# Kernel tuning notes

Measured on AMD Instinct MI355X. Metric: run time of the kernel, lower is better.

Reference implementation:

```python
import jax, jax.numpy as jnp
import numpy as np

N, M, FIN, FOUT, K = 16, 20000, 64, 64, 6
NNZ = 160000


def setup_inputs() -> dict:
    key = jax.random.key(0)
    k1, k2, k3, k4, k5, k6 = jax.random.split(key, 6)
    x = jax.random.normal(k1, (N, M, FIN), dtype=jnp.float32)
    # sparse Laplacian in COO form; small values keep the Chebyshev recurrence stable
    L_vals = jax.random.normal(k2, (NNZ,), dtype=jnp.float32) * 0.05
    L_rows = jax.random.randint(k3, (NNZ,), 0, M, dtype=jnp.int32)
    L_cols = jax.random.randint(k4, (NNZ,), 0, M, dtype=jnp.int32)
    stdv = 1.0 / np.sqrt(FOUT)
    weight = jax.random.uniform(k5, (FIN * K, FOUT), dtype=jnp.float32, minval=-stdv, maxval=stdv)
    bias = jax.random.uniform(k6, (FOUT,), dtype=jnp.float32, minval=-stdv, maxval=stdv)
    return {"x": x, "L_vals": L_vals, "weight": weight, "bias": bias,
            "L_rows": L_rows, "L_cols": L_cols}


def reference(x, L_vals, weight, bias, L_rows, L_cols):
    n, m, fin = x.shape
    # x0: [M, Fin*N], matching torch permute(1,2,0).view(M, Fin*N)
    x0 = jnp.transpose(x, (1, 2, 0)).reshape(m, fin * n)

    def spmm(v):  # sparse [M,M] @ dense [M, Fin*N]
        return jax.ops.segment_sum(L_vals[:, None] * v[L_cols], L_rows, num_segments=m)

    terms = [x0]
    if K > 1:
        x1 = spmm(x0)
        terms.append(x1)
    xk_2, xk_1 = x0, x1
    for _ in range(2, K):
        xk = 2.0 * spmm(xk_1) - xk_2
        terms.append(xk)
        xk_2, xk_1 = xk_1, xk

    xs = jnp.stack(terms, axis=0)                       # [K, M, Fin*N]
    xs = xs.reshape(K, m, fin, n)
    xs = jnp.transpose(xs, (3, 1, 2, 0)).reshape(n * m, fin * K)
    out = xs @ weight + bias                            # [N*M, Fout]
    return out.reshape(n, m, -1)
```

## Files before the change

### kernel.cpp

```cpp
#include <hip/hip_runtime.h>
#include <hip/hip_bf16.h>
#include <hip/hip_fp16.h>

#define NB 16
#define MB 20000
#define FINC 64
#define FOUTC 64
#define KCH 6
#define NNZC 160000
#define CW 1024
#define ELLW 32

typedef __attribute__((ext_vector_type(8))) short short8;
typedef __attribute__((ext_vector_type(4))) float float4v;
typedef __attribute__((ext_vector_type(4))) unsigned int ui4;

__device__ inline unsigned short f2bf(float f){
  unsigned int u = __float_as_uint(f);
  u += 0x7FFFu + ((u >> 16) & 1u);
  return (unsigned short)(u >> 16);
}
__device__ inline float bflo(unsigned int u){ return __uint_as_float(u << 16); }
__device__ inline float bfhi(unsigned int u){ return __uint_as_float(u & 0xFFFF0000u); }
__device__ inline float h2f(unsigned int bits){
  __half_raw hr; hr.x = (unsigned short)bits;
  return __half2float(*(__half*)&hr);
}

__global__ void k_build(const int* __restrict__ rows, const int* __restrict__ cols,
                        const float* __restrict__ vals,
                        int* __restrict__ cnt, unsigned int* __restrict__ ell){
  int i = blockIdx.x * 256 + threadIdx.x;
  if (i < NNZC){
    int r = rows[i];
    int slot = atomicAdd(&cnt[r], 1);
    if (slot < ELLW){
      __half h = __float2half(vals[i]);
      __half_raw hr = *(__half_raw*)&h;
      unsigned int entry = (unsigned int)(unsigned short)cols[i] | ((unsigned int)hr.x << 16);
      ell[r * ELLW + slot] = entry;
    }
  }
}

__global__ void __launch_bounds__(256) k_prep(const float* __restrict__ x,
                                              const float* __restrict__ w,
                                              unsigned short* __restrict__ G0,
                                              unsigned short* __restrict__ W2t){
  int b = blockIdx.x;
  if (b < 1250){
    int t = threadIdx.x;
    int m = b * 16 + (t >> 4);
    int fc = (t & 15) * 4;
    #pragma unroll
    for (int n = 0; n < NB; n++){
      float4 a = *(const float4*)(x + ((size_t)n * MB + m) * FINC + fc);
      unsigned short tmp[4] = {f2bf(a.x), f2bf(a.y), f2bf(a.z), f2bf(a.w)};
      *(uint2*)(G0 + (size_t)m * CW + n * FINC + fc) = *(const uint2*)tmp;
    }
  } else {
    int idx = (b - 1250) * 256 + threadIdx.x;
    if (idx < KCH * FINC * FOUTC){
      int k  = idx / (FINC * FOUTC);
      int fo = (idx / FINC) % FOUTC;
      int f  = idx % FINC;
      W2t[idx] = f2bf(w[(f * KCH + k) * FOUTC + fo]);
    }
  }
}

__device__ inline void gacc(float* acc, ui4 raw, float v){
  acc[0] += v * bflo(raw.x); acc[1] += v * bfhi(raw.x);
  acc[2] += v * bflo(raw.y); acc[3] += v * bfhi(raw.y);
  acc[4] += v * bflo(raw.z); acc[5] += v * bfhi(raw.z);
  acc[6] += v * bflo(raw.w); acc[7] += v * bfhi(raw.w);
}

__global__ void __launch_bounds__(128) k_spmm(const unsigned short* __restrict__ Gin,
                                              const unsigned short* __restrict__ Gprev,
                                              unsigned short* __restrict__ Gout,
                                              const int* __restrict__ cnt,
                                              const unsigned int* __restrict__ ell,
                                              int first){
  int bid = blockIdx.x;
  int xcd   = bid & 7;
  int t2    = bid >> 3;
  int phase = t2 / 1250;
  int mg    = t2 - phase * 1250;
  int slab  = xcd + 8 * phase;
  int t = threadIdx.x;
  int m = mg * 16 + (t >> 3);
  int co = slab * 64 + (t & 7) * 8;
  int deg = cnt[m]; if (deg > ELLW) deg = ELLW;

  const ui4* ep4 = (const ui4*)(ell + m * ELLW);
  ui4 q0 = ep4[0];
  ui4 q1 = ep4[1];
  ui4 pr = (ui4){0u,0u,0u,0u};
  if (!first) pr = *(const ui4*)(Gprev + (size_t)m * CW + co);

  const unsigned short* gb = Gin + co;
  ui4 r0 = *(const ui4*)(gb + (size_t)(q0.x & 0xFFFFu) * CW);
  ui4 r1 = *(const ui4*)(gb + (size_t)(q0.y & 0xFFFFu) * CW);
  ui4 r2 = *(const ui4*)(gb + (size_t)(q0.z & 0xFFFFu) * CW);
  ui4 r3 = *(const ui4*)(gb + (size_t)(q0.w & 0xFFFFu) * CW);
  ui4 r4 = *(const ui4*)(gb + (size_t)(q1.x & 0xFFFFu) * CW);
  ui4 r5 = *(const ui4*)(gb + (size_t)(q1.y & 0xFFFFu) * CW);
  ui4 r6 = *(const ui4*)(gb + (size_t)(q1.z & 0xFFFFu) * CW);
  ui4 r7 = *(const ui4*)(gb + (size_t)(q1.w & 0xFFFFu) * CW);

  float acc[8] = {0.f,0.f,0.f,0.f,0.f,0.f,0.f,0.f};
  gacc(acc, r0, h2f(q0.x >> 16));
  gacc(acc, r1, h2f(q0.y >> 16));
  gacc(acc, r2, h2f(q0.z >> 16));
  gacc(acc, r3, h2f(q0.w >> 16));
  gacc(acc, r4, h2f(q1.x >> 16));
  gacc(acc, r5, h2f(q1.y >> 16));
  gacc(acc, r6, h2f(q1.z >> 16));
  gacc(acc, r7, h2f(q1.w >> 16));

  if (deg > 8){
    for (int e = 8; e < deg; e += 8){
      ui4 a0 = ep4[e >> 2];
      ui4 a1 = ep4[(e >> 2) + 1];
      ui4 s0 = *(const ui4*)(gb + (size_t)(a0.x & 0xFFFFu) * CW);
      ui4 s1 = *(const ui4*)(gb + (size_t)(a0.y & 0xFFFFu) * CW);
      ui4 s2 = *(const ui4*)(gb + (size_t)(a0.z & 0xFFFFu) * CW);
      ui4 s3 = *(const ui4*)(gb + (size_t)(a0.w & 0xFFFFu) * CW);
      ui4 s4 = *(const ui4*)(gb + (size_t)(a1.x & 0xFFFFu) * CW);
      ui4 s5 = *(const ui4*)(gb + (size_t)(a1.y & 0xFFFFu) * CW);
      ui4 s6 = *(const ui4*)(gb + (size_t)(a1.z & 0xFFFFu) * CW);
      ui4 s7 = *(const ui4*)(gb + (size_t)(a1.w & 0xFFFFu) * CW);
      gacc(acc, s0, h2f(a0.x >> 16));
      gacc(acc, s1, h2f(a0.y >> 16));
      gacc(acc, s2, h2f(a0.z >> 16));
      gacc(acc, s3, h2f(a0.w >> 16));
      gacc(acc, s4, h2f(a1.x >> 16));
      gacc(acc, s5, h2f(a1.y >> 16));
      gacc(acc, s6, h2f(a1.z >> 16));
      gacc(acc, s7, h2f(a1.w >> 16));
    }
  }

  if (!first){
    float pv[8] = {bflo(pr.x), bfhi(pr.x), bflo(pr.y), bfhi(pr.y),
                   bflo(pr.z), bfhi(pr.z), bflo(pr.w), bfhi(pr.w)};
    #pragma unroll
    for (int i = 0; i < 8; i++) acc[i] = 2.f * acc[i] - pv[i];
  }
  unsigned short o[8];
  #pragma unroll
  for (int i = 0; i < 8; i++) o[i] = f2bf(acc[i]);
  *(ui4*)(Gout + (size_t)m * CW + co) = *(const ui4*)o;
}

#define LDA 72
__global__ void __launch_bounds__(256, 2) k_gemm(const unsigned short* __restrict__ G,
                                                 const unsigned short* __restrict__ W2t,
                                                 const float* __restrict__ bias,
                                                 float* __restrict__ out){
  __shared__ unsigned short la[128 * LDA];
  __shared__ unsigned short lb[FOUTC * LDA];
  int tid  = threadIdx.x;
  int wave = tid >> 6, lane = tid & 63;
  int quad = lane >> 4, l16 = lane & 15;
  int mblk = blockIdx.x;
  const size_t gsz = (size_t)MB * CW;

  float4v acc[2][4];
  #pragma unroll
  for (int i = 0; i < 2; i++)
    #pragma unroll
    for (int j = 0; j < 4; j++) acc[i][j] = (float4v){0.f, 0.f, 0.f, 0.f};

  const unsigned short* a0p = G + (size_t)mblk * 8 * CW;
  uint4 ra0 = *(const uint4*)(a0p + (0 * 256 + tid) * 8);
  uint4 ra1 = *(const uint4*)(a0p + (1 * 256 + tid) * 8);
  uint4 ra2 = *(const uint4*)(a0p + (2 * 256 + tid) * 8);
  uint4 ra3 = *(const uint4*)(a0p + (3 * 256 + tid) * 8);
  uint4 rb0 = *(const uint4*)(W2t + (0 * 256 + tid) * 8);
  uint4 rb1 = *(const uint4*)(W2t + (1 * 256 + tid) * 8);

  for (int k = 0; k < KCH; k++){
    __syncthreads();
    {
      int e0;
      e0 = (0 * 256 + tid) * 8; *(uint4*)(&la[(e0 >> 6) * LDA + (e0 & 63)]) = ra0;
      e0 = (1 * 256 + tid) * 8; *(uint4*)(&la[(e0 >> 6) * LDA + (e0 & 63)]) = ra1;
      e0 = (2 * 256 + tid) * 8; *(uint4*)(&la[(e0 >> 6) * LDA + (e0 & 63)]) = ra2;
      e0 = (3 * 256 + tid) * 8; *(uint4*)(&la[(e0 >> 6) * LDA + (e0 & 63)]) = ra3;
      e0 = (0 * 256 + tid) * 8; *(uint4*)(&lb[(e0 >> 6) * LDA + (e0 & 63)]) = rb0;
      e0 = (1 * 256 + tid) * 8; *(uint4*)(&lb[(e0 >> 6) * LDA + (e0 & 63)]) = rb1;
    }
    __syncthreads();
    int kn = (k + 1 < KCH) ? k + 1 : k;
    const unsigned short* an = G + (size_t)kn * gsz + (size_t)mblk * 8 * CW;
    const unsigned short* bn = W2t + kn * (FINC * FOUTC);
    uint4 na0 = *(const uint4*)(an + (0 * 256 + tid) * 8);
    uint4 na1 = *(const uint4*)(an + (1 * 256 + tid) * 8);
    uint4 na2 = *(const uint4*)(an + (2 * 256 + tid) * 8);
    uint4 na3 = *(const uint4*)(an + (3 * 256 + tid) * 8);
    uint4 nb0 = *(const uint4*)(bn + (0 * 256 + tid) * 8);
    uint4 nb1 = *(const uint4*)(bn + (1 * 256 + tid) * 8);

    #pragma unroll
    for (int kc = 0; kc < 2; kc++){
      short8 af[2], bfr[4];
      #pragma unroll
      for (int rt = 0; rt < 2; rt++){
        int row = wave * 32 + rt * 16 + l16;
        af[rt] = *(const short8*)(&la[row * LDA + kc * 32 + quad * 8]);
      }
      #pragma unroll
      for (int ct = 0; ct < 4; ct++){
        int fo = ct * 16 + l16;
        bfr[ct] = *(const short8*)(&lb[fo * LDA + kc * 32 + quad * 8]);
      }
      #pragma unroll
      for (int rt = 0; rt < 2; rt++)
        #pragma unroll
        for (int ct = 0; ct < 4; ct++)
          acc[rt][ct] = __builtin_amdgcn_mfma_f32_16x16x32_bf16(af[rt], bfr[ct], acc[rt][ct], 0, 0, 0);
    }
    ra0 = na0; ra1 = na1; ra2 = na2; ra3 = na3; rb0 = nb0; rb1 = nb1;
  }
  #pragma unroll
  for (int ct = 0; ct < 4; ct++){
    int fo = ct * 16 + l16;
    float bv = bias[fo];
    #pragma unroll
    for (int rt = 0; rt < 2; rt++){
      #pragma unroll
      for (int reg = 0; reg < 4; reg++){
        int rloc = wave * 32 + rt * 16 + quad * 4 + reg;
        int r = mblk * 128 + rloc;
        int m = r >> 4, n = r & 15;
        out[((size_t)n * MB + m) * FOUTC + fo] = acc[rt][ct][reg] + bv;
      }
    }
  }
}

extern "C" void kernel_launch(void* const* d_in, const int* in_sizes, int n_in,
                              void* d_out, int out_size, void* d_ws, size_t ws_size,
                              hipStream_t stream){
  const float* x    = (const float*)d_in[0];
  const float* Lv   = (const float*)d_in[1];
  const float* w    = (const float*)d_in[2];
  const float* bias = (const float*)d_in[3];
  const int*   Lr   = (const int*)d_in[4];
  const int*   Lc   = (const int*)d_in[5];
  float* out = (float*)d_out;

  char* ws = (char*)d_ws;
  unsigned short* G   = (unsigned short*)ws;
  unsigned short* W2t = (unsigned short*)(ws + 245760000);
  int* cnt            = (int*)(ws + 245809152);
  unsigned int* ell = (unsigned int*)d_out;

  (void)hipMemsetAsync(cnt, 0, MB * sizeof(int), stream);
  (void)hipMemsetAsync(ell, 0, MB * ELLW * sizeof(unsigned int), stream);

  k_build<<<dim3((NNZC + 255) / 256), dim3(256), 0, stream>>>(Lr, Lc, Lv, cnt, ell);
  k_prep <<<dim3(1250 + 96), dim3(256), 0, stream>>>(x, w, G, W2t);

  const size_t gsz = (size_t)MB * CW;
  k_spmm<<<dim3(1250 * 16), dim3(128), 0, stream>>>(G, (const unsigned short*)nullptr, G + gsz,
                                                    cnt, ell, 1);
  for (int k = 2; k < KCH; k++)
    k_spmm<<<dim3(1250 * 16), dim3(128), 0, stream>>>(G + (size_t)(k - 1) * gsz, G + (size_t)(k - 2) * gsz,
                                                      G + (size_t)k * gsz, cnt, ell, 0);

  k_gemm<<<dim3(MB / 8), dim3(256), 0, stream>>>(G, W2t, bias, out);
}
```

Measured before the change: 397.3 us.

## Loop over column slabs per block in SpMM and stage ELL entries in LDS

The SpMM kernel drops from 20000 blocks (one per row group and column slab, with XCD-aware slab mapping) to 1250 blocks that each loop over all 16 column slabs. Each block loads its rows' ELL entries into shared memory once, pre-decoding byte offsets and fp16 values, so the index and value decode is amortised across slabs. The cost is far fewer blocks (1250 of 128 threads) and a serialised slab loop, which reduces parallelism and latency hiding. It also removes the XCD-based mapping that kept slabs local to L2.

```diff
diff --git a/kernel.cpp b/kernel.cpp
--- a/kernel.cpp
+++ b/kernel.cpp
@@ -82,76 +82,89 @@
                                               const int* __restrict__ cnt,
                                               const unsigned int* __restrict__ ell,
                                               int first){
-  int bid = blockIdx.x;
-  int xcd   = bid & 7;
-  int t2    = bid >> 3;
-  int phase = t2 / 1250;
-  int mg    = t2 - phase * 1250;
-  int slab  = xcd + 8 * phase;
-  int t = threadIdx.x;
-  int m = mg * 16 + (t >> 3);
-  int co = slab * 64 + (t & 7) * 8;
+  __shared__ unsigned int loff[16 * ELLW];
+  __shared__ float        lval[16 * ELLW];
+  int blk = blockIdx.x;
+  int t   = threadIdx.x;
+  int r   = t >> 3;
+  int m   = blk * 16 + r;
+  int cth = t & 7;
+
+  {
+    ui4 e = ((const ui4*)(ell + blk * 16 * ELLW))[t];
+    int base = t * 4;
+    loff[base + 0] = (e.x & 0xFFFFu) * (CW * 2); lval[base + 0] = h2f(e.x >> 16);
+    loff[base + 1] = (e.y & 0xFFFFu) * (CW * 2); lval[base + 1] = h2f(e.y >> 16);
+    loff[base + 2] = (e.z & 0xFFFFu) * (CW * 2); lval[base + 2] = h2f(e.z >> 16);
+    loff[base + 3] = (e.w & 0xFFFFu) * (CW * 2); lval[base + 3] = h2f(e.w >> 16);
+  }
   int deg = cnt[m]; if (deg > ELLW) deg = ELLW;
-
-  const ui4* ep4 = (const ui4*)(ell + m * ELLW);
-  ui4 q0 = ep4[0];
-  ui4 q1 = ep4[1];
-  ui4 pr = (ui4){0u,0u,0u,0u};
-  if (!first) pr = *(const ui4*)(Gprev + (size_t)m * CW + co);
-
-  const unsigned short* gb = Gin + co;
-  ui4 r0 = *(const ui4*)(gb + (size_t)(q0.x & 0xFFFFu) * CW);
-  ui4 r1 = *(const ui4*)(gb + (size_t)(q0.y & 0xFFFFu) * CW);
-  ui4 r2 = *(const ui4*)(gb + (size_t)(q0.z & 0xFFFFu) * CW);
-  ui4 r3 = *(const ui4*)(gb + (size_t)(q0.w & 0xFFFFu) * CW);
-  ui4 r4 = *(const ui4*)(gb + (size_t)(q1.x & 0xFFFFu) * CW);
-  ui4 r5 = *(const ui4*)(gb + (size_t)(q1.y & 0xFFFFu) * CW);
-  ui4 r6 = *(const ui4*)(gb + (size_t)(q1.z & 0xFFFFu) * CW);
-  ui4 r7 = *(const ui4*)(gb + (size_t)(q1.w & 0xFFFFu) * CW);
-
-  float acc[8] = {0.f,0.f,0.f,0.f,0.f,0.f,0.f,0.f};
-  gacc(acc, r0, h2f(q0.x >> 16));
-  gacc(acc, r1, h2f(q0.y >> 16));
-  gacc(acc, r2, h2f(q0.z >> 16));
-  gacc(acc, r3, h2f(q0.w >> 16));
-  gacc(acc, r4, h2f(q1.x >> 16));
-  gacc(acc, r5, h2f(q1.y >> 16));
-  gacc(acc, r6, h2f(q1.z >> 16));
-  gacc(acc, r7, h2f(q1.w >> 16));
-
-  if (deg > 8){
-    for (int e = 8; e < deg; e += 8){
-      ui4 a0 = ep4[e >> 2];
-      ui4 a1 = ep4[(e >> 2) + 1];
-      ui4 s0 = *(const ui4*)(gb + (size_t)(a0.x & 0xFFFFu) * CW);
-      ui4 s1 = *(const ui4*)(gb + (size_t)(a0.y & 0xFFFFu) * CW);
-      ui4 s2 = *(const ui4*)(gb + (size_t)(a0.z & 0xFFFFu) * CW);
-      ui4 s3 = *(const ui4*)(gb + (size_t)(a0.w & 0xFFFFu) * CW);
-      ui4 s4 = *(const ui4*)(gb + (size_t)(a1.x & 0xFFFFu) * CW);
-      ui4 s5 = *(const ui4*)(gb + (size_t)(a1.y & 0xFFFFu) * CW);
-      ui4 s6 = *(const ui4*)(gb + (size_t)(a1.z & 0xFFFFu) * CW);
-      ui4 s7 = *(const ui4*)(gb + (size_t)(a1.w & 0xFFFFu) * CW);
-      gacc(acc, s0, h2f(a0.x >> 16));
-      gacc(acc, s1, h2f(a0.y >> 16));
-      gacc(acc, s2, h2f(a0.z >> 16));
-      gacc(acc, s3, h2f(a0.w >> 16));
-      gacc(acc, s4, h2f(a1.x >> 16));
-      gacc(acc, s5, h2f(a1.y >> 16));
-      gacc(acc, s6, h2f(a1.z >> 16));
-      gacc(acc, s7, h2f(a1.w >> 16));
-    }
-  }
-
-  if (!first){
-    float pv[8] = {bflo(pr.x), bfhi(pr.x), bflo(pr.y), bfhi(pr.y),
-                   bflo(pr.z), bfhi(pr.z), bflo(pr.w), bfhi(pr.w)};
-    #pragma unroll
-    for (int i = 0; i < 8; i++) acc[i] = 2.f * acc[i] - pv[i];
-  }
-  unsigned short o[8];
-  #pragma unroll
-  for (int i = 0; i < 8; i++) o[i] = f2bf(acc[i]);
-  *(ui4*)(Gout + (size_t)m * CW + co) = *(const ui4*)o;
+  __syncthreads();
+
+  const ui4*    offs4 = (const ui4*)&loff[r * ELLW];
+  const float4* vals4 = (const float4*)&lval[r * ELLW];
+
+  for (int s = 0; s < 16; s++){
+    int co = s * 64 + cth * 8;
+    const char* gb = (const char*)Gin + (size_t)co * 2;
+    ui4 pr = (ui4){0u,0u,0u,0u};
+    if (!first) pr = *(const ui4*)(Gprev + (size_t)m * CW + co);
+
+    ui4 oa = offs4[0], ob = offs4[1];
+    float4 va = vals4[0], vb = vals4[1];
+    ui4 r0 = *(const ui4*)(gb + oa.x);
+    ui4 r1 = *(const ui4*)(gb + oa.y);
+    ui4 r2 = *(const ui4*)(gb + oa.z);
+    ui4 r3 = *(const ui4*)(gb + oa.w);
+    ui4 r4 = *(const ui4*)(gb + ob.x);
+    ui4 r5 = *(const ui4*)(gb + ob.y);
+    ui4 r6 = *(const ui4*)(gb + ob.z);
+    ui4 r7 = *(const ui4*)(gb + ob.w);
+
+    float acc[8] = {0.f,0.f,0.f,0.f,0.f,0.f,0.f,0.f};
+    gacc(acc, r0, va.x);
+    gacc(acc, r1, va.y);
+    gacc(acc, r2, va.z);
+    gacc(acc, r3, va.w);
+    gacc(acc, r4, vb.x);
+    gacc(acc, r5, vb.y);
+    gacc(acc, r6, vb.z);
+    gacc(acc, r7, vb.w);
+
+    if (deg > 8){
+      for (int e = 8; e < deg; e += 8){
+        ui4 pa = offs4[e >> 2], pb = offs4[(e >> 2) + 1];
+        float4 wa = vals4[e >> 2], wb = vals4[(e >> 2) + 1];
+        ui4 s0 = *(const ui4*)(gb + pa.x);
+        ui4 s1 = *(const ui4*)(gb + pa.y);
+        ui4 s2 = *(const ui4*)(gb + pa.z);
+        ui4 s3 = *(const ui4*)(gb + pa.w);
+        ui4 s4 = *(const ui4*)(gb + pb.x);
+        ui4 s5 = *(const ui4*)(gb + pb.y);
+        ui4 s6 = *(const ui4*)(gb + pb.z);
+        ui4 s7 = *(const ui4*)(gb + pb.w);
+        gacc(acc, s0, wa.x);
+        gacc(acc, s1, wa.y);
+        gacc(acc, s2, wa.z);
+        gacc(acc, s3, wa.w);
+        gacc(acc, s4, wb.x);
+        gacc(acc, s5, wb.y);
+        gacc(acc, s6, wb.z);
+        gacc(acc, s7, wb.w);
+      }
+    }
+
+    if (!first){
+      float pv[8] = {bflo(pr.x), bfhi(pr.x), bflo(pr.y), bfhi(pr.y),
+                     bflo(pr.z), bfhi(pr.z), bflo(pr.w), bfhi(pr.w)};
+      #pragma unroll
+      for (int i = 0; i < 8; i++) acc[i] = 2.f * acc[i] - pv[i];
+    }
+    unsigned short o[8];
+    #pragma unroll
+    for (int i = 0; i < 8; i++) o[i] = f2bf(acc[i]);
+    *(ui4*)(Gout + (size_t)m * CW + co) = *(const ui4*)o;
+  }
 }
 
 #define LDA 72
@@ -265,11 +278,11 @@
   k_prep <<<dim3(1250 + 96), dim3(256), 0, stream>>>(x, w, G, W2t);
 
   const size_t gsz = (size_t)MB * CW;
-  k_spmm<<<dim3(1250 * 16), dim3(128), 0, stream>>>(G, (const unsigned short*)nullptr, G + gsz,
-                                                    cnt, ell, 1);
+  k_spmm<<<dim3(1250), dim3(128), 0, stream>>>(G, (const unsigned short*)nullptr, G + gsz,
+                                               cnt, ell, 1);
   for (int k = 2; k < KCH; k++)
-    k_spmm<<<dim3(1250 * 16), dim3(128), 0, stream>>>(G + (size_t)(k - 1) * gsz, G + (size_t)(k - 2) * gsz,
-                                                      G + (size_t)k * gsz, cnt, ell, 0);
+    k_spmm<<<dim3(1250), dim3(128), 0, stream>>>(G + (size_t)(k - 1) * gsz, G + (size_t)(k - 2) * gsz,
+                                                 G + (size_t)k * gsz, cnt, ell, 0);
 
   k_gemm<<<dim3(MB / 8), dim3(256), 0, stream>>>(G, W2t, bias, out);
 }
```

Measured after the change: 490.9 us. 23.6% more time.
